# Kernel tuning notes

Hardware: AMD Instinct MI355X
Metric: run time of the kernel (lower is better)

The kernel has to match this reference:

```python
import jax, jax.numpy as jnp
import numpy as np

EPS = 1e-6

def _rms_norm(x, w):
    # normalize over last dim (head_dim)
    var = jnp.mean(jnp.square(x), axis=-1, keepdims=True)
    return x * jax.lax.rsqrt(var + EPS) * w

def _rotate_half(x):
    half = x.shape[-1] // 2
    first, second = x[..., :half], x[..., half:]
    return jnp.concatenate([-second, first], axis=-1)

def _apply_rope(x, cos, sin):
    # x: [B,H,S,D]; cos/sin: [B,S,D] -> broadcast over heads
    return x * cos[:, None] + _rotate_half(x) * sin[:, None]

def setup_inputs() -> dict:
    key = jax.random.key(0)
    ks = jax.random.split(key, 10)
    B, Sq, Sk, Dm, H = 2, 2048, 2048, 2048, 16
    hd = Dm // H
    scale = 1.0 / np.sqrt(Dm)
    return {
        "x": jax.random.normal(ks[0], (B, Sq, Dm), jnp.float32),
        "context": jax.random.normal(ks[1], (B, Sk, Dm), jnp.float32),
        "cos_q": jax.random.uniform(ks[2], (B, Sq, hd), jnp.float32),
        "sin_q": jax.random.uniform(ks[3], (B, Sq, hd), jnp.float32),
        "cos_k": jax.random.uniform(ks[4], (B, Sk, hd), jnp.float32),
        "sin_k": jax.random.uniform(ks[5], (B, Sk, hd), jnp.float32),
        "Wq": jax.random.normal(ks[6], (Dm, Dm), jnp.float32) * scale,
        "Wk": jax.random.normal(ks[7], (Dm, Dm), jnp.float32) * scale,
        "Wv": jax.random.normal(ks[8], (Dm, Dm), jnp.float32) * scale,
        "Wo": jax.random.normal(ks[9], (Dm, Dm), jnp.float32) * scale,
        "q_norm_w": jnp.ones((hd,), jnp.float32),
        "k_norm_w": jnp.ones((hd,), jnp.float32),
    }

def reference(x, context, cos_q, sin_q, cos_k, sin_k, Wq, Wk, Wv, Wo, q_norm_w, k_norm_w):
    B, Sq, Dm = x.shape
    hd = q_norm_w.shape[0]
    H = Dm // hd
    # projections (torch Linear: y = x @ W.T), reshape to [B,H,S,D]
    q = (x @ Wq.T).reshape(B, Sq, H, hd).transpose(0, 2, 1, 3)
    k = (context @ Wk.T).reshape(B, -1, H, hd).transpose(0, 2, 1, 3)
    v = (context @ Wv.T).reshape(B, -1, H, hd).transpose(0, 2, 1, 3)
    # per-head QK RMSNorm
    q = _rms_norm(q, q_norm_w)
    k = _rms_norm(k, k_norm_w)
    # RoPE
    q = _apply_rope(q, cos_q, sin_q)
    k = _apply_rope(k, cos_k, sin_k)
    # SDPA, scale = 1/sqrt(head_dim)
    scale = 1.0 / np.sqrt(hd).astype(np.float32)
    scores = jnp.einsum('bhqd,bhkd->bhqk', q, k) * scale
    attn = jax.nn.softmax(scores, axis=-1)
    y = jnp.einsum('bhqk,bhkd->bhqd', attn, v)
    y = y.transpose(0, 2, 1, 3).reshape(B, Sq, Dm)
    return y @ Wo.T
```

## Files before the change

### kernel.cpp

```cpp
#include <hip/hip_runtime.h>


typedef __attribute__((ext_vector_type(8))) short bf16x8;
typedef __attribute__((ext_vector_type(4))) float f32x4;

#define AS1(p) ((__attribute__((address_space(1))) void*)(p))
#define AS3(p) ((__attribute__((address_space(3))) void*)(p))

__device__ __forceinline__ unsigned short f2bf(float f) {
  unsigned int u = __float_as_uint(f);
  u += 0x7fffu + ((u >> 16) & 1u);
  return (unsigned short)(u >> 16);
}

constexpr int B_ = 2, S_ = 2048, DM = 2048, H_ = 16, HD = 128;
constexpr int M_ = B_ * S_;

__global__ __launch_bounds__(256) void castbf(const float* __restrict__ X,
                                              unsigned short* __restrict__ Y, int n4) {
  int i = blockIdx.x * 256 + threadIdx.x;
  if (i >= n4) return;
  float4 v = ((const float4*)X)[i];
  ushort4 u;
  u.x = f2bf(v.x); u.y = f2bf(v.y); u.z = f2bf(v.z); u.w = f2bf(v.w);
  ((ushort4*)Y)[i] = u;
}

__global__ __launch_bounds__(256) void gemm_bt(const unsigned short* __restrict__ A,
                                               const unsigned short* __restrict__ Bw,
                                               float* __restrict__ C,
                                               int M, int N, int K) {
  __shared__ unsigned short lA[128 * 32];
  __shared__ unsigned short lB[128 * 32];
  const int tid = threadIdx.x, wave = tid >> 6, lane = tid & 63;
  const int quad = lane >> 4, l16 = lane & 15;
  const int m0 = blockIdx.x * 128, n0 = blockIdx.y * 128;
  const int wm = (wave >> 1) * 64, wn = (wave & 1) * 64;
  f32x4 acc[4][4];
#pragma unroll
  for (int i = 0; i < 4; i++)
#pragma unroll
    for (int j = 0; j < 4; j++) acc[i][j] = (f32x4){0.f, 0.f, 0.f, 0.f};

  for (int k0 = 0; k0 < K; k0 += 32) {
    __syncthreads();
#pragma unroll
    for (int call = 0; call < 2; ++call) {
      int c = wave * 128 + call * 64 + lane;
      int row = c >> 2, s = c & 3;
      int dc = s ^ ((row >> 1) & 3);
      __builtin_amdgcn_global_load_lds(AS1(A + (size_t)(m0 + row) * K + k0 + dc * 8),
                                       AS3(lA + (wave * 128 + call * 64) * 8), 16, 0, 0);
      __builtin_amdgcn_global_load_lds(AS1(Bw + (size_t)(n0 + row) * K + k0 + dc * 8),
                                       AS3(lB + (wave * 128 + call * 64) * 8), 16, 0, 0);
    }
    __syncthreads();

    bf16x8 af[4], bfr[4];
#pragma unroll
    for (int i = 0; i < 4; i++) {
      int r = wm + i * 16 + l16;
      af[i] = *(const bf16x8*)(lA + r * 32 + (quad ^ ((r >> 1) & 3)) * 8);
      int cN = wn + i * 16 + l16;
      bfr[i] = *(const bf16x8*)(lB + cN * 32 + (quad ^ ((cN >> 1) & 3)) * 8);
    }
#pragma unroll
    for (int i = 0; i < 4; i++)
#pragma unroll
      for (int j = 0; j < 4; j++)
        acc[i][j] = __builtin_amdgcn_mfma_f32_16x16x32_bf16(af[i], bfr[j], acc[i][j], 0, 0, 0);
  }
#pragma unroll
  for (int i = 0; i < 4; i++)
#pragma unroll
    for (int j = 0; j < 4; j++) {
      float* cp = C + (size_t)(m0 + wm + i * 16 + quad * 4) * N + (n0 + wn + j * 16 + l16);
#pragma unroll
      for (int r = 0; r < 4; r++) cp[(size_t)r * N] = acc[i][j][r];
    }
}

__global__ __launch_bounds__(256) void normrope(const float* __restrict__ X,
                                                const float* __restrict__ Cs,
                                                const float* __restrict__ Sn,
                                                const float* __restrict__ W,
                                                unsigned short* __restrict__ Out,
                                                float scale) {
  int gw = (blockIdx.x * 256 + threadIdx.x) >> 6;
  int lane = threadIdx.x & 63;
  int h = gw & 15, bs = gw >> 4;
  int s = bs & (S_ - 1), b = bs >> 11;
  const float* xr = X + (size_t)gw * HD;
  float x0 = xr[lane], x1 = xr[lane + 64];
  float ss = x0 * x0 + x1 * x1;
#pragma unroll
  for (int off = 32; off > 0; off >>= 1) ss += __shfl_xor(ss, off);
  float rr = rsqrtf(ss * (1.0f / 128.0f) + 1e-6f);
  float n0 = x0 * rr * W[lane], n1 = x1 * rr * W[lane + 64];
  const float* cp = Cs + (size_t)bs * HD;
  const float* sp = Sn + (size_t)bs * HD;
  float o0 = (n0 * cp[lane] - n1 * sp[lane]) * scale;
  float o1 = (n1 * cp[lane + 64] + n0 * sp[lane + 64]) * scale;
  unsigned short* orow = Out + (((size_t)(b * H_ + h)) * S_ + s) * HD;
  orow[lane] = f2bf(o0);
  orow[lane + 64] = f2bf(o1);
}

__global__ __launch_bounds__(256) void vtrans(const float* __restrict__ Vf,
                                              unsigned short* __restrict__ Vt) {
  __shared__ unsigned short tile[128 * 72];
  const int tid = threadIdx.x;
  const int sc = blockIdx.x & 31;
  const int bh = blockIdx.x >> 5;
  const int b = bh >> 4, h = bh & 15;
  const int s0 = sc * 64;
#pragma unroll
  for (int it = 0; it < 8; ++it) {
    int ci = it * 256 + tid;
    int s = ci >> 5, dq = ci & 31;
    float4 v = *(const float4*)(Vf + ((size_t)(b * S_ + s0 + s)) * DM + h * HD + dq * 4);
    unsigned short* tp = tile + (dq * 4) * 72 + s;
    tp[0] = f2bf(v.x); tp[72] = f2bf(v.y); tp[144] = f2bf(v.z); tp[216] = f2bf(v.w);
  }
  __syncthreads();
#pragma unroll
  for (int it = 0; it < 4; ++it) {
    int cj = it * 256 + tid;
    int d = cj >> 3, scx = cj & 7;
    bf16x8 vv = *(const bf16x8*)(tile + d * 72 + scx * 8);
    *(bf16x8*)(Vt + ((size_t)bh * HD + d) * S_ + s0 + scx * 8) = vv;
  }
}

__global__ __launch_bounds__(256) void flash(const unsigned short* __restrict__ Q,
                                             const unsigned short* __restrict__ Kt,
                                             const unsigned short* __restrict__ Vt,
                                             unsigned short* __restrict__ Y) {
  __shared__ unsigned short lK[32 * HD];
  __shared__ unsigned short lV[HD * 32];
  __shared__ unsigned short lP[4 * 16 * 32];
  const int tid = threadIdx.x, wave = tid >> 6, lane = tid & 63;
  const int quad = lane >> 4, l16 = lane & 15;
  const int qb = blockIdx.x & 31;
  const int bh = blockIdx.x >> 5;
  const int b = bh >> 4, h = bh & 15;
  const int q0 = qb * 64 + wave * 16;

  bf16x8 aq[4];
  {
    const unsigned short* qrow = Q + ((size_t)bh * S_ + q0 + l16) * HD;
#pragma unroll
    for (int t = 0; t < 4; t++) aq[t] = *(const bf16x8*)(qrow + t * 32 + quad * 8);
  }
  f32x4 o[8];
#pragma unroll
  for (int t = 0; t < 8; t++) o[t] = (f32x4){0.f, 0.f, 0.f, 0.f};
  float lsum[4] = {0.f, 0.f, 0.f, 0.f};

  const unsigned short* kbase = Kt + (size_t)bh * S_ * HD;
  const unsigned short* vbase = Vt + (size_t)bh * HD * S_;
  unsigned short* lPw = lP + wave * 512;
  const int mrow = quad * 4;
  const int xsl = (l16 >> 1) & 3;

  for (int k0 = 0; k0 < S_; k0 += 32) {
    __syncthreads();
#pragma unroll
    for (int call = 0; call < 2; ++call) {
      int c = wave * 128 + call * 64 + lane;
      int key = c >> 4, sk = c & 15;
      int dck = sk ^ (key & 15);
      __builtin_amdgcn_global_load_lds(AS1(kbase + (size_t)(k0 + key) * HD + dck * 8),
                                       AS3(lK + (wave * 128 + call * 64) * 8), 16, 0, 0);
      int dv = c >> 2, sv = c & 3;
      int kc = sv ^ ((dv >> 1) & 3);
      __builtin_amdgcn_global_load_lds(AS1(vbase + (size_t)dv * S_ + k0 + kc * 8),
                                       AS3(lV + (wave * 128 + call * 64) * 8), 16, 0, 0);
    }
    __syncthreads();

    f32x4 sacc0 = (f32x4){0.f, 0.f, 0.f, 0.f}, sacc1 = (f32x4){0.f, 0.f, 0.f, 0.f};
    {
      const unsigned short* krow0 = lK + l16 * HD;
      const unsigned short* krow1 = lK + (16 + l16) * HD;
#pragma unroll
      for (int t = 0; t < 4; t++) {
        int dcq = t * 4 + quad;
        bf16x8 kf0 = *(const bf16x8*)(krow0 + (dcq ^ l16) * 8);
        sacc0 = __builtin_amdgcn_mfma_f32_16x16x32_bf16(aq[t], kf0, sacc0, 0, 0, 0);
        bf16x8 kf1 = *(const bf16x8*)(krow1 + (dcq ^ l16) * 8);
        sacc1 = __builtin_amdgcn_mfma_f32_16x16x32_bf16(aq[t], kf1, sacc1, 0, 0, 0);
      }
    }
#pragma unroll
    for (int r = 0; r < 4; r++) {
      int m = mrow + r;
      int sx = (m >> 1) & 3;
      float p0 = __expf(sacc0[r]);
      float p1 = __expf(sacc1[r]);
      lsum[r] += p0 + p1;
      int kc0 = l16 >> 3;
      lPw[m * 32 + ((kc0 ^ sx)) * 8 + (l16 & 7)] = f2bf(p0);
      lPw[m * 32 + (((kc0 + 2) ^ sx)) * 8 + (l16 & 7)] = f2bf(p1);
    }
    bf16x8 pf = *(const bf16x8*)(lPw + l16 * 32 + (quad ^ xsl) * 8);
#pragma unroll
    for (int t = 0; t < 8; t++) {
      bf16x8 vf = *(const bf16x8*)(lV + (t * 16 + l16) * 32 + (quad ^ xsl) * 8);
      o[t] = __builtin_amdgcn_mfma_f32_16x16x32_bf16(pf, vf, o[t], 0, 0, 0);
    }
  }

#pragma unroll
  for (int off = 1; off < 16; off <<= 1) {
#pragma unroll
    for (int r = 0; r < 4; r++) lsum[r] += __shfl_xor(lsum[r], off);
  }
  float inv[4];
#pragma unroll
  for (int r = 0; r < 4; r++) inv[r] = 1.0f / lsum[r];
#pragma unroll
  for (int t = 0; t < 8; t++)
#pragma unroll
    for (int r = 0; r < 4; r++) {
      size_t idx = ((size_t)b * S_ + q0 + mrow + r) * DM + h * HD + t * 16 + l16;
      Y[idx] = f2bf(o[t][r] * inv[r]);
    }
}

extern "C" void kernel_launch(void* const* d_in, const int* in_sizes, int n_in,
                              void* d_out, int out_size, void* d_ws, size_t ws_size,
                              hipStream_t stream) {
  const float* x    = (const float*)d_in[0];
  const float* ctx  = (const float*)d_in[1];
  const float* cosq = (const float*)d_in[2];
  const float* sinq = (const float*)d_in[3];
  const float* cosk = (const float*)d_in[4];
  const float* sink = (const float*)d_in[5];
  const float* Wq   = (const float*)d_in[6];
  const float* Wk   = (const float*)d_in[7];
  const float* Wv   = (const float*)d_in[8];
  const float* Wo   = (const float*)d_in[9];
  const float* qw   = (const float*)d_in[10];
  const float* kw   = (const float*)d_in[11];

  char* ws = (char*)d_ws;
  const size_t ACT2 = (size_t)M_ * DM * 2;
  const size_t W2   = (size_t)DM * DM * 2;
  unsigned short* xb  = (unsigned short*)(ws);
  unsigned short* cb  = (unsigned short*)(ws + ACT2);
  unsigned short* Wqb = (unsigned short*)(ws + 2 * ACT2);
  unsigned short* Wkb = (unsigned short*)(ws + 2 * ACT2 + W2);
  unsigned short* Wvb = (unsigned short*)(ws + 2 * ACT2 + 2 * W2);
  unsigned short* Wob = (unsigned short*)(ws + 2 * ACT2 + 3 * W2);
  float*          Pf  = (float*)(ws + 2 * ACT2 + 4 * W2);
  unsigned short* qn = xb;
  unsigned short* kn = Wqb;
  unsigned short* vt = cb;
  unsigned short* yb = (unsigned short*)Pf;

  const float scale = 0.0883883476483184f;
  dim3 gg(M_ / 128, DM / 128);

  castbf<<<M_ * DM / 1024, 256, 0, stream>>>(x, xb, M_ * DM / 4);
  castbf<<<M_ * DM / 1024, 256, 0, stream>>>(ctx, cb, M_ * DM / 4);
  castbf<<<DM * DM / 1024, 256, 0, stream>>>(Wq, Wqb, DM * DM / 4);
  castbf<<<DM * DM / 1024, 256, 0, stream>>>(Wk, Wkb, DM * DM / 4);
  castbf<<<DM * DM / 1024, 256, 0, stream>>>(Wv, Wvb, DM * DM / 4);
  castbf<<<DM * DM / 1024, 256, 0, stream>>>(Wo, Wob, DM * DM / 4);

  gemm_bt<<<gg, 256, 0, stream>>>(xb, Wqb, Pf, M_, DM, DM);
  normrope<<<M_ * H_ / 4, 256, 0, stream>>>(Pf, cosq, sinq, qw, qn, scale);

  gemm_bt<<<gg, 256, 0, stream>>>(cb, Wkb, Pf, M_, DM, DM);
  normrope<<<M_ * H_ / 4, 256, 0, stream>>>(Pf, cosk, sink, kw, kn, 1.0f);

  gemm_bt<<<gg, 256, 0, stream>>>(cb, Wvb, Pf, M_, DM, DM);
  vtrans<<<B_ * H_ * (S_ / 64), 256, 0, stream>>>(Pf, vt);

  flash<<<B_ * H_ * (S_ / 64), 256, 0, stream>>>(qn, kn, vt, yb);

  gemm_bt<<<gg, 256, 0, stream>>>(yb, Wob, (float*)d_out, M_, DM, DM);

  (void)in_sizes; (void)n_in; (void)out_size; (void)ws_size;
}
```

Measured before the change: 551.2 us.

## Process two 16-row query tiles per wave in flash attention to reuse K/V fragments

Each wave now handles 32 query rows (two 16-row MFMA tiles) instead of 16, so each block covers 128 queries and the grid halves. Every K and V fragment read from LDS, and every K/V tile loaded from global memory, now feeds twice as many MFMAs, which reduces LDS and global traffic per unit of work. In exchange, accumulator register use doubles, which may lower occupancy, and the grid drops to 512 blocks, which reduces parallelism across CUs.

```diff
diff --git a/kernel.cpp b/kernel.cpp
--- a/kernel.cpp
+++ b/kernel.cpp
@@ -138,28 +138,31 @@
                                              unsigned short* __restrict__ Y) {
   __shared__ unsigned short lK[32 * HD];
   __shared__ unsigned short lV[HD * 32];
-  __shared__ unsigned short lP[4 * 16 * 32];
+  __shared__ unsigned short lP[4 * 32 * 32];
   const int tid = threadIdx.x, wave = tid >> 6, lane = tid & 63;
   const int quad = lane >> 4, l16 = lane & 15;
-  const int qb = blockIdx.x & 31;
-  const int bh = blockIdx.x >> 5;
+  const int qb = blockIdx.x & 15;
+  const int bh = blockIdx.x >> 4;
   const int b = bh >> 4, h = bh & 15;
-  const int q0 = qb * 64 + wave * 16;
-
-  bf16x8 aq[4];
-  {
-    const unsigned short* qrow = Q + ((size_t)bh * S_ + q0 + l16) * HD;
-#pragma unroll
-    for (int t = 0; t < 4; t++) aq[t] = *(const bf16x8*)(qrow + t * 32 + quad * 8);
-  }
-  f32x4 o[8];
-#pragma unroll
-  for (int t = 0; t < 8; t++) o[t] = (f32x4){0.f, 0.f, 0.f, 0.f};
-  float lsum[4] = {0.f, 0.f, 0.f, 0.f};
+  const int q0 = qb * 128 + wave * 32;
+
+  bf16x8 aq[2][4];
+#pragma unroll
+  for (int u = 0; u < 2; u++) {
+    const unsigned short* qrow = Q + ((size_t)bh * S_ + q0 + u * 16 + l16) * HD;
+#pragma unroll
+    for (int t = 0; t < 4; t++) aq[u][t] = *(const bf16x8*)(qrow + t * 32 + quad * 8);
+  }
+  f32x4 o[2][8];
+#pragma unroll
+  for (int u = 0; u < 2; u++)
+#pragma unroll
+    for (int t = 0; t < 8; t++) o[u][t] = (f32x4){0.f, 0.f, 0.f, 0.f};
+  float lsum[2][4] = {{0.f, 0.f, 0.f, 0.f}, {0.f, 0.f, 0.f, 0.f}};
 
   const unsigned short* kbase = Kt + (size_t)bh * S_ * HD;
   const unsigned short* vbase = Vt + (size_t)bh * HD * S_;
-  unsigned short* lPw = lP + wave * 512;
+  unsigned short* lPw = lP + wave * 1024;
   const int mrow = quad * 4;
   const int xsl = (l16 >> 1) & 3;
 
@@ -179,7 +182,8 @@
     }
     __syncthreads();
 
-    f32x4 sacc0 = (f32x4){0.f, 0.f, 0.f, 0.f}, sacc1 = (f32x4){0.f, 0.f, 0.f, 0.f};
+    f32x4 s0[2] = {(f32x4){0.f, 0.f, 0.f, 0.f}, (f32x4){0.f, 0.f, 0.f, 0.f}};
+    f32x4 s1[2] = {(f32x4){0.f, 0.f, 0.f, 0.f}, (f32x4){0.f, 0.f, 0.f, 0.f}};
     {
       const unsigned short* krow0 = lK + l16 * HD;
       const unsigned short* krow1 = lK + (16 + l16) * HD;
@@ -187,45 +191,63 @@
       for (int t = 0; t < 4; t++) {
         int dcq = t * 4 + quad;
         bf16x8 kf0 = *(const bf16x8*)(krow0 + (dcq ^ l16) * 8);
-        sacc0 = __builtin_amdgcn_mfma_f32_16x16x32_bf16(aq[t], kf0, sacc0, 0, 0, 0);
         bf16x8 kf1 = *(const bf16x8*)(krow1 + (dcq ^ l16) * 8);
-        sacc1 = __builtin_amdgcn_mfma_f32_16x16x32_bf16(aq[t], kf1, sacc1, 0, 0, 0);
+#pragma unroll
+        for (int u = 0; u < 2; u++) {
+          s0[u] = __builtin_amdgcn_mfma_f32_16x16x32_bf16(aq[u][t], kf0, s0[u], 0, 0, 0);
+          s1[u] = __builtin_amdgcn_mfma_f32_16x16x32_bf16(aq[u][t], kf1, s1[u], 0, 0, 0);
+        }
       }
     }
 #pragma unroll
-    for (int r = 0; r < 4; r++) {
-      int m = mrow + r;
-      int sx = (m >> 1) & 3;
-      float p0 = __expf(sacc0[r]);
-      float p1 = __expf(sacc1[r]);
-      lsum[r] += p0 + p1;
-      int kc0 = l16 >> 3;
-      lPw[m * 32 + ((kc0 ^ sx)) * 8 + (l16 & 7)] = f2bf(p0);
-      lPw[m * 32 + (((kc0 + 2) ^ sx)) * 8 + (l16 & 7)] = f2bf(p1);
-    }
-    bf16x8 pf = *(const bf16x8*)(lPw + l16 * 32 + (quad ^ xsl) * 8);
+    for (int u = 0; u < 2; u++) {
+      unsigned short* lPu = lPw + u * 512;
+#pragma unroll
+      for (int r = 0; r < 4; r++) {
+        int m = mrow + r;
+        int sx = (m >> 1) & 3;
+        float p0 = __expf(s0[u][r]);
+        float p1 = __expf(s1[u][r]);
+        lsum[u][r] += p0 + p1;
+        int kc0 = l16 >> 3;
+        lPu[m * 32 + ((kc0 ^ sx)) * 8 + (l16 & 7)] = f2bf(p0);
+        lPu[m * 32 + (((kc0 + 2) ^ sx)) * 8 + (l16 & 7)] = f2bf(p1);
+      }
+    }
+    bf16x8 pf[2];
+#pragma unroll
+    for (int u = 0; u < 2; u++)
+      pf[u] = *(const bf16x8*)(lPw + u * 512 + l16 * 32 + (quad ^ xsl) * 8);
 #pragma unroll
     for (int t = 0; t < 8; t++) {
       bf16x8 vf = *(const bf16x8*)(lV + (t * 16 + l16) * 32 + (quad ^ xsl) * 8);
-      o[t] = __builtin_amdgcn_mfma_f32_16x16x32_bf16(pf, vf, o[t], 0, 0, 0);
+#pragma unroll
+      for (int u = 0; u < 2; u++)
+        o[u][t] = __builtin_amdgcn_mfma_f32_16x16x32_bf16(pf[u], vf, o[u][t], 0, 0, 0);
     }
   }
 
 #pragma unroll
   for (int off = 1; off < 16; off <<= 1) {
 #pragma unroll
-    for (int r = 0; r < 4; r++) lsum[r] += __shfl_xor(lsum[r], off);
-  }
-  float inv[4];
-#pragma unroll
-  for (int r = 0; r < 4; r++) inv[r] = 1.0f / lsum[r];
-#pragma unroll
-  for (int t = 0; t < 8; t++)
-#pragma unroll
-    for (int r = 0; r < 4; r++) {
-      size_t idx = ((size_t)b * S_ + q0 + mrow + r) * DM + h * HD + t * 16 + l16;
-      Y[idx] = f2bf(o[t][r] * inv[r]);
-    }
+    for (int u = 0; u < 2; u++)
+#pragma unroll
+      for (int r = 0; r < 4; r++) lsum[u][r] += __shfl_xor(lsum[u][r], off);
+  }
+  float inv[2][4];
+#pragma unroll
+  for (int u = 0; u < 2; u++)
+#pragma unroll
+    for (int r = 0; r < 4; r++) inv[u][r] = 1.0f / lsum[u][r];
+#pragma unroll
+  for (int u = 0; u < 2; u++)
+#pragma unroll
+    for (int t = 0; t < 8; t++)
+#pragma unroll
+      for (int r = 0; r < 4; r++) {
+        size_t idx = ((size_t)b * S_ + q0 + u * 16 + mrow + r) * DM + h * HD + t * 16 + l16;
+        Y[idx] = f2bf(o[u][t][r] * inv[u][r]);
+      }
 }
 
 extern "C" void kernel_launch(void* const* d_in, const int* in_sizes, int n_in,
@@ -278,7 +300,7 @@
   gemm_bt<<<gg, 256, 0, stream>>>(cb, Wvb, Pf, M_, DM, DM);
   vtrans<<<B_ * H_ * (S_ / 64), 256, 0, stream>>>(Pf, vt);
 
-  flash<<<B_ * H_ * (S_ / 64), 256, 0, stream>>>(qn, kn, vt, yb);
+  flash<<<B_ * H_ * (S_ / 128), 256, 0, stream>>>(qn, kn, vt, yb);
 
   gemm_bt<<<gg, 256, 0, stream>>>(yb, Wob, (float*)d_out, M_, DM, DM);
 
```

After: 561.6 us. No clear change (+1.9%).
